# Optimization experiments

Measured on AMD Instinct MI355X. Metric: run time of the kernel, lower is better.

The kernel has to match this reference:

```python
import jax, jax.numpy as jnp
import numpy as np
import math

B, S, D, H = 2, 2048, 1024, 16
DH = D // H
DFF = 4 * D
EPS = 1e-6


def layer_norm(x, g, b):
    # Faithful to the torch module: std is Bessel-corrected (ddof=1) and eps is
    # added to std (not variance).
    mean = jnp.mean(x, axis=-1, keepdims=True)
    var = jnp.sum((x - mean) ** 2, axis=-1, keepdims=True) / (x.shape[-1] - 1)
    return g * (x - mean) / (jnp.sqrt(var) + EPS) + b


def gelu_tanh(h):
    c = math.sqrt(2.0 / math.pi)
    return 0.5 * h * (1.0 + jnp.tanh(c * (h + 0.044715 * h ** 3)))


def attention(x, mask, wq, bq, wk, bk, wv, bv, wo, bo):
    b, s, d = x.shape
    q = (x @ wq + bq).reshape(b, s, H, DH)
    k = (x @ wk + bk).reshape(b, s, H, DH)
    v = (x @ wv + bv).reshape(b, s, H, DH)
    corr = jnp.einsum('bqhd,bkhd->bhqk', q, k) / math.sqrt(DH)  # [B,H,S,S]
    # original builds mask[:,None,:].repeat -> key-axis padding mask
    corr = jnp.where(mask[:, None, None, :] == 0, jnp.float32(-1e9), corr)
    prob = jax.nn.softmax(corr, axis=-1)
    hid = jnp.einsum('bhqk,bkhd->bqhd', prob, v).reshape(b, s, d)
    return hid @ wo + bo


def setup_inputs() -> dict:
    key = jax.random.key(0)
    ks = jax.random.split(key, 16)
    std = 0.02
    inp = {
        'hidden': jax.random.normal(ks[0], (B, S, D), jnp.float32),
        'mask': jax.random.randint(ks[1], (B, S), 0, 2, jnp.int32),
        'wq': jax.random.normal(ks[2], (D, D), jnp.float32) * std,
        'bq': jnp.zeros((D,), jnp.float32),
        'wk': jax.random.normal(ks[3], (D, D), jnp.float32) * std,
        'bk': jnp.zeros((D,), jnp.float32),
        'wv': jax.random.normal(ks[4], (D, D), jnp.float32) * std,
        'bv': jnp.zeros((D,), jnp.float32),
        'wo': jax.random.normal(ks[5], (D, D), jnp.float32) * std,
        'bo': jnp.zeros((D,), jnp.float32),
        'w1': jax.random.normal(ks[6], (D, DFF), jnp.float32) * std,
        'b1': jnp.zeros((DFF,), jnp.float32),
        'w2': jax.random.normal(ks[7], (DFF, D), jnp.float32) * std,
        'b2': jnp.zeros((D,), jnp.float32),
        'ln1_g': jnp.ones((D,), jnp.float32),
        'ln1_b': jnp.zeros((D,), jnp.float32),
        'ln2_g': jnp.ones((D,), jnp.float32),
        'ln2_b': jnp.zeros((D,), jnp.float32),
    }
    return inp


def reference(hidden, mask, wq, bq, wk, bk, wv, bv, wo, bo, w1, b1, w2, b2,
              ln1_g, ln1_b, ln2_g, ln2_b):
    # pre-norm residual attention sublayer (dropout = identity in eval)
    h = hidden + attention(layer_norm(hidden, ln1_g, ln1_b), mask,
                           wq, bq, wk, bk, wv, bv, wo, bo)
    # pre-norm residual FFN sublayer with tanh-GELU
    ff_in = layer_norm(h, ln2_g, ln2_b)
    h = h + (gelu_tanh(ff_in @ w1 + b1) @ w2 + b2)
    return h
```

## Files before the change

### kernel.cpp

```cpp
#include <hip/hip_runtime.h>

#define BB 2
#define SS 2048
#define DD 1024
#define HH 16
#define DHH 64
#define DFF 4096
#define MM (BB * SS)

typedef unsigned short u16;
typedef short short8 __attribute__((ext_vector_type(8)));
typedef float f32x4 __attribute__((ext_vector_type(4)));

__device__ __forceinline__ float b2f(u16 u) {
    return __uint_as_float(((unsigned)u) << 16);
}
__device__ __forceinline__ u16 f2b(float f) {
    unsigned u = __float_as_uint(f);
    unsigned r = (u + 0x7fffu + ((u >> 16) & 1u)) >> 16;
    return (u16)r;
}
__device__ __forceinline__ float gelu_tanh_f(float x) {
    float x3 = x * x * x;
    float t = 0.7978845608028654f * (x + 0.044715f * x3);
    return 0.5f * x * (1.0f + tanhf(t));
}

__global__ __launch_bounds__(256) void wconv(const float* __restrict__ W,
                                             u16* __restrict__ WT,
                                             int Kdim, int Ndim) {
    __shared__ float tile[64][65];
    const int t = threadIdx.x;
    const int k0 = blockIdx.x * 64, n0 = blockIdx.y * 64;
    const int c = t & 63, r0 = (t >> 6) * 16;
#pragma unroll
    for (int i = 0; i < 16; ++i)
        tile[r0 + i][c] = W[(size_t)(k0 + r0 + i) * Ndim + n0 + c];
    __syncthreads();
    const int k4 = (t & 15) * 4, nr = t >> 4;
#pragma unroll
    for (int i = 0; i < 4; ++i) {
        int n = nr + 16 * i;
        ushort4 u = {f2b(tile[k4 + 0][n]), f2b(tile[k4 + 1][n]),
                     f2b(tile[k4 + 2][n]), f2b(tile[k4 + 3][n])};
        *(ushort4*)&WT[(size_t)(n0 + n) * Kdim + k0 + k4] = u;
    }
}

template <typename TI>
__global__ __launch_bounds__(256) void ln_kernel(const TI* __restrict__ x,
                                                 const float* __restrict__ g,
                                                 const float* __restrict__ bb,
                                                 u16* __restrict__ out) {
    __shared__ float red[8];
    const int row = blockIdx.x;
    const int t = threadIdx.x;
    const size_t base = (size_t)row * DD;

    float xv[4];
#pragma unroll
    for (int i = 0; i < 4; ++i) {
        int j = t + i * 256;
        if constexpr (sizeof(TI) == 2) xv[i] = b2f(((const u16*)x)[base + j]);
        else                            xv[i] = ((const float*)x)[base + j];
    }

    float part = xv[0] + xv[1] + xv[2] + xv[3];
#pragma unroll
    for (int off = 32; off > 0; off >>= 1) part += __shfl_xor(part, off);
    if ((t & 63) == 0) red[t >> 6] = part;
    __syncthreads();
    const float mean = (red[0] + red[1] + red[2] + red[3]) * (1.0f / 1024.0f);

    float dv[4];
#pragma unroll
    for (int i = 0; i < 4; ++i) dv[i] = xv[i] - mean;
    float p2 = dv[0] * dv[0] + dv[1] * dv[1] + dv[2] * dv[2] + dv[3] * dv[3];
#pragma unroll
    for (int off = 32; off > 0; off >>= 1) p2 += __shfl_xor(p2, off);
    if ((t & 63) == 0) red[4 + (t >> 6)] = p2;
    __syncthreads();
    const float var = (red[4] + red[5] + red[6] + red[7]) * (1.0f / 1023.0f);
    const float rden = 1.0f / (sqrtf(var) + 1e-6f);

#pragma unroll
    for (int i = 0; i < 4; ++i) {
        int j = t + i * 256;
        out[base + j] = f2b(g[j] * dv[i] * rden + bb[j]);
    }
}

template <int EPI>
__device__ __forceinline__ void gemm_store(int row, int col, float v,
                                           const void* res, void* out, int Ndim) {
    if (EPI == 0 || EPI == 4) {
        if (EPI == 4) v *= 0.125f;
        const int bq = row >> 11, ss = row & 2047;
        const int hh = col >> 6, dh = col & 63;
        ((u16*)out)[(((size_t)bq * HH + hh) * SS + ss) * DHH + dh] = f2b(v);
    } else if (EPI == 1) {
        const size_t o = (size_t)row * Ndim + col;
        ((u16*)out)[o] = f2b(v + ((const float*)res)[o]);
    } else if (EPI == 2) {
        ((u16*)out)[(size_t)row * Ndim + col] = f2b(gelu_tanh_f(v));
    } else {
        const size_t o = (size_t)row * Ndim + col;
        ((float*)out)[o] = v + b2f(((const u16*)res)[o]);
    }
}

template <int EPI, int TM>
__global__ __launch_bounds__(256) void gemm_bb(const u16* __restrict__ A,
                                               const u16* __restrict__ BTg,
                                               const float* __restrict__ bias,
                                               const void* __restrict__ res,
                                               void* __restrict__ out,
                                               int Ndim, int Kdim) {
    constexpr int NI = (TM == 128) ? 4 : 2;
    __shared__ __align__(16) u16 As[TM * 64];
    __shared__ __align__(16) u16 Bs[128 * 64];

    const int t = threadIdx.x;
    const int w = t >> 6, l = t & 63;
    const int lm = l & 15, lg = l >> 4;
    const int m0 = blockIdx.y * TM, n0 = blockIdx.x * 128;
    const int wro = (TM == 128) ? (w >> 1) * 64 : 0;
    const int wco = (TM == 128) ? (w & 1) * 64 : w * 32;

    f32x4 acc[4][NI];
#pragma unroll
    for (int mi = 0; mi < 4; ++mi)
#pragma unroll
        for (int ni = 0; ni < NI; ++ni) acc[mi][ni] = (f32x4){0.f, 0.f, 0.f, 0.f};

    for (int k0 = 0; k0 < Kdim; k0 += 64) {
#pragma unroll
        for (int it = 0; it < TM / 32; ++it) {
            int idx = it * 256 + t;
            int row = idx >> 3, c8 = (idx & 7) * 8;
            short8 v = *(const short8*)(A + (size_t)(m0 + row) * Kdim + k0 + c8);
            *(short8*)&As[row * 64 + (c8 ^ ((row & 7) * 8))] = v;
        }
#pragma unroll
        for (int it = 0; it < 4; ++it) {
            int idx = it * 256 + t;
            int row = idx >> 3, c8 = (idx & 7) * 8;
            short8 v = *(const short8*)(BTg + (size_t)(n0 + row) * Kdim + k0 + c8);
            *(short8*)&Bs[row * 64 + (c8 ^ ((row & 7) * 8))] = v;
        }
        __syncthreads();

#pragma unroll
        for (int ks = 0; ks < 64; ks += 32) {
            short8 af[4], bf[NI];
#pragma unroll
            for (int mi = 0; mi < 4; ++mi) {
                const int row = wro + mi * 16 + lm;
                af[mi] = *(const short8*)&As[row * 64 + ((ks + lg * 8) ^ ((row & 7) * 8))];
            }
#pragma unroll
            for (int ni = 0; ni < NI; ++ni) {
                const int nn = wco + ni * 16 + lm;
                bf[ni] = *(const short8*)&Bs[nn * 64 + ((ks + lg * 8) ^ ((nn & 7) * 8))];
            }
#pragma unroll
            for (int mi = 0; mi < 4; ++mi)
#pragma unroll
                for (int ni = 0; ni < NI; ++ni)
                    acc[mi][ni] = __builtin_amdgcn_mfma_f32_16x16x32_bf16(
                        af[mi], bf[ni], acc[mi][ni], 0, 0, 0);
        }
        __syncthreads();
    }

#pragma unroll
    for (int ni = 0; ni < NI; ++ni) {
        const int col = n0 + wco + ni * 16 + lm;
        const float bv = bias[col];
#pragma unroll
        for (int mi = 0; mi < 4; ++mi)
#pragma unroll
            for (int r = 0; r < 4; ++r)
                gemm_store<EPI>(m0 + wro + mi * 16 + lg * 4 + r, col,
                                acc[mi][ni][r] + bv, res, out, Ndim);
    }
}

template <int EPI, int TM>
__global__ __launch_bounds__(256) void gemm_fb(const u16* __restrict__ A,
                                               const float* __restrict__ W,
                                               const float* __restrict__ bias,
                                               const void* __restrict__ res,
                                               void* __restrict__ out,
                                               int Ndim, int Kdim) {
    constexpr int NI = (TM == 128) ? 4 : 2;
    __shared__ __align__(16) u16 As[TM * 64];
    __shared__ __align__(16) u16 BT[128 * 64];

    const int t = threadIdx.x;
    const int w = t >> 6, l = t & 63;
    const int lm = l & 15, lg = l >> 4;
    const int m0 = blockIdx.y * TM, n0 = blockIdx.x * 128;
    const int wro = (TM == 128) ? (w >> 1) * 64 : 0;
    const int wco = (TM == 128) ? (w & 1) * 64 : w * 32;

    f32x4 acc[4][NI];
#pragma unroll
    for (int mi = 0; mi < 4; ++mi)
#pragma unroll
        for (int ni = 0; ni < NI; ++ni) acc[mi][ni] = (f32x4){0.f, 0.f, 0.f, 0.f};

    const int bn = t & 127;
    const int bk4 = (t >> 7) * 4;

    for (int k0 = 0; k0 < Kdim; k0 += 64) {
#pragma unroll
        for (int it = 0; it < TM / 32; ++it) {
            int idx = it * 256 + t;
            int row = idx >> 3, c8 = (idx & 7) * 8;
            short8 v = *(const short8*)(A + (size_t)(m0 + row) * Kdim + k0 + c8);
            *(short8*)&As[row * 64 + (c8 ^ ((row & 7) * 8))] = v;
        }
#pragma unroll
        for (int it = 0; it < 8; ++it) {
            int kq = it * 8 + bk4;
            const float* wp = W + (size_t)(k0 + kq) * Ndim + n0 + bn;
            ushort4 u = {f2b(wp[0]), f2b(wp[(size_t)Ndim]),
                         f2b(wp[2 * (size_t)Ndim]), f2b(wp[3 * (size_t)Ndim])};
            *(ushort4*)&BT[bn * 64 + (kq ^ ((bn & 7) * 8))] = u;
        }
        __syncthreads();

#pragma unroll
        for (int ks = 0; ks < 64; ks += 32) {
            short8 af[4], bf[NI];
#pragma unroll
            for (int mi = 0; mi < 4; ++mi) {
                const int row = wro + mi * 16 + lm;
                af[mi] = *(const short8*)&As[row * 64 + ((ks + lg * 8) ^ ((row & 7) * 8))];
            }
#pragma unroll
            for (int ni = 0; ni < NI; ++ni) {
                const int nn = wco + ni * 16 + lm;
                bf[ni] = *(const short8*)&BT[nn * 64 + ((ks + lg * 8) ^ ((nn & 7) * 8))];
            }
#pragma unroll
            for (int mi = 0; mi < 4; ++mi)
#pragma unroll
                for (int ni = 0; ni < NI; ++ni)
                    acc[mi][ni] = __builtin_amdgcn_mfma_f32_16x16x32_bf16(
                        af[mi], bf[ni], acc[mi][ni], 0, 0, 0);
        }
        __syncthreads();
    }

#pragma unroll
    for (int ni = 0; ni < NI; ++ni) {
        const int col = n0 + wco + ni * 16 + lm;
        const float bv = bias[col];
#pragma unroll
        for (int mi = 0; mi < 4; ++mi)
#pragma unroll
            for (int r = 0; r < 4; ++r)
                gemm_store<EPI>(m0 + wro + mi * 16 + lg * 4 + r, col,
                                acc[mi][ni][r] + bv, res, out, Ndim);
    }
}

__global__ __launch_bounds__(256) void attn_mfma2(const u16* __restrict__ qg,
                                                  const u16* __restrict__ kg,
                                                  const u16* __restrict__ vg,
                                                  const int* __restrict__ mask,
                                                  u16* __restrict__ hid) {
    __shared__ __align__(16) u16 Ks[64 * 72];
    __shared__ __align__(16) u16 VTs[64 * 72];
    __shared__ __align__(16) float maskf[64];

    const int t = threadIdx.x;
    const int w = t >> 6;
    const int l = t & 63;
    const int lm = l & 15, lg = l >> 4;
    const int h = blockIdx.y, b = blockIdx.z;
    const int qbase = blockIdx.x * 128 + w * 32;
    const size_t bhS = ((size_t)b * HH + h) * SS;

    short8 qlo[2], qhi[2];
#pragma unroll
    for (int qp = 0; qp < 2; ++qp) {
        const u16* qrow = qg + (bhS + qbase + qp * 16 + lm) * DHH + lg * 8;
        qlo[qp] = *(const short8*)qrow;
        qhi[qp] = *(const short8*)(qrow + 32);
    }

    f32x4 acc[2][4];
#pragma unroll
    for (int qp = 0; qp < 2; ++qp)
#pragma unroll
        for (int i = 0; i < 4; ++i) acc[qp][i] = (f32x4){0.f, 0.f, 0.f, 0.f};
    float sume[2] = {0.f, 0.f};

    const int kq = (t & 15) * 4, dq = (t >> 4) * 4;

    for (int kt = 0; kt < SS; kt += 64) {
        __syncthreads();
#pragma unroll
        for (int it = 0; it < 4; ++it) {
            int idx = it * 256 + t;
            int row = idx >> 4, c4 = (idx & 15) * 4;
            ushort4 u = *(const ushort4*)(kg + (bhS + kt + row) * DHH + c4);
            *(ushort4*)&Ks[row * 72 + c4] = u;
        }
        {
            ushort4 a0 = *(const ushort4*)(vg + (bhS + kt + kq + 0) * DHH + dq);
            ushort4 a1 = *(const ushort4*)(vg + (bhS + kt + kq + 1) * DHH + dq);
            ushort4 a2 = *(const ushort4*)(vg + (bhS + kt + kq + 2) * DHH + dq);
            ushort4 a3 = *(const ushort4*)(vg + (bhS + kt + kq + 3) * DHH + dq);
            ushort4 w0 = {a0.x, a1.x, a2.x, a3.x};
            ushort4 w1 = {a0.y, a1.y, a2.y, a3.y};
            ushort4 w2 = {a0.z, a1.z, a2.z, a3.z};
            ushort4 w3 = {a0.w, a1.w, a2.w, a3.w};
            *(ushort4*)&VTs[(dq + 0) * 72 + kq] = w0;
            *(ushort4*)&VTs[(dq + 1) * 72 + kq] = w1;
            *(ushort4*)&VTs[(dq + 2) * 72 + kq] = w2;
            *(ushort4*)&VTs[(dq + 3) * 72 + kq] = w3;
        }
        if (t < 64) maskf[t] = mask[b * SS + kt + t] ? 1.0f : 0.0f;
        __syncthreads();

#pragma unroll
        for (int kb = 0; kb < 64; kb += 32) {
            short8 kfa[2], kfc[2];
#pragma unroll
            for (int s = 0; s < 2; ++s) {
                const int keyrow = kb + 8 * (lm >> 2) + 4 * s + (lm & 3);
                const u16* kr = &Ks[keyrow * 72 + lg * 8];
                kfa[s] = *(const short8*)kr;
                kfc[s] = *(const short8*)(kr + 32);
            }
            short8 p8[2];
#pragma unroll
            for (int qp = 0; qp < 2; ++qp) {
                float ev[8];
#pragma unroll
                for (int s = 0; s < 2; ++s) {
                    f32x4 c = (f32x4){0.f, 0.f, 0.f, 0.f};
                    c = __builtin_amdgcn_mfma_f32_16x16x32_bf16(kfa[s], qlo[qp], c, 0, 0, 0);
                    c = __builtin_amdgcn_mfma_f32_16x16x32_bf16(kfc[s], qhi[qp], c, 0, 0, 0);
                    const float4 mv = *(const float4*)&maskf[kb + 8 * lg + 4 * s];
                    float e0 = __expf(c[0]) * mv.x;
                    float e1 = __expf(c[1]) * mv.y;
                    float e2 = __expf(c[2]) * mv.z;
                    float e3 = __expf(c[3]) * mv.w;
                    sume[qp] += e0 + e1 + e2 + e3;
                    ev[4 * s + 0] = e0; ev[4 * s + 1] = e1;
                    ev[4 * s + 2] = e2; ev[4 * s + 3] = e3;
                }
#pragma unroll
                for (int i = 0; i < 8; ++i) p8[qp][i] = (short)f2b(ev[i]);
            }
#pragma unroll
            for (int d0 = 0; d0 < 4; ++d0) {
                const short8 v8 = *(const short8*)&VTs[(d0 * 16 + lm) * 72 + kb + lg * 8];
#pragma unroll
                for (int qp = 0; qp < 2; ++qp)
                    acc[qp][d0] = __builtin_amdgcn_mfma_f32_16x16x32_bf16(
                        p8[qp], v8, acc[qp][d0], 0, 0, 0);
            }
        }
    }

#pragma unroll
    for (int qp = 0; qp < 2; ++qp) {
        float s = sume[qp];
        s += __shfl_xor(s, 16);
        s += __shfl_xor(s, 32);
        float rinv[4];
#pragma unroll
        for (int r = 0; r < 4; ++r) rinv[r] = 1.0f / __shfl(s, 4 * lg + r);
#pragma unroll
        for (int d0 = 0; d0 < 4; ++d0)
#pragma unroll
            for (int r = 0; r < 4; ++r) {
                const int q = qbase + qp * 16 + 4 * lg + r;
                hid[(size_t)(b * SS + q) * DD + h * DHH + d0 * 16 + lm] =
                    f2b(acc[qp][d0][r] * rinv[r]);
            }
    }
}

extern "C" void kernel_launch(void* const* d_in, const int* in_sizes, int n_in,
                              void* d_out, int out_size, void* d_ws, size_t ws_size,
                              hipStream_t stream) {
    (void)in_sizes; (void)n_in; (void)out_size;

    const float* hidden = (const float*)d_in[0];
    const int*   mask   = (const int*)d_in[1];
    const float* wq = (const float*)d_in[2];  const float* bq = (const float*)d_in[3];
    const float* wk = (const float*)d_in[4];  const float* bk = (const float*)d_in[5];
    const float* wv = (const float*)d_in[6];  const float* bv = (const float*)d_in[7];
    const float* wo = (const float*)d_in[8];  const float* bo = (const float*)d_in[9];
    const float* w1 = (const float*)d_in[10]; const float* b1 = (const float*)d_in[11];
    const float* w2 = (const float*)d_in[12]; const float* b2 = (const float*)d_in[13];
    const float* ln1g = (const float*)d_in[14]; const float* ln1b = (const float*)d_in[15];
    const float* ln2g = (const float*)d_in[16]; const float* ln2b = (const float*)d_in[17];

    char* ws = (char*)d_ws;
    u16* R0 = (u16*)(ws + 0);
    u16* R1 = (u16*)(ws + 8388608);
    u16* R2 = (u16*)(ws + 16777216);
    u16* R3 = (u16*)(ws + 25165824);
    float* outp = (float*)d_out;

    const size_t WTOFF = 33554432;
    const bool big = ws_size >= WTOFF + 25165824;

    if (big) {
        u16* wqT = (u16*)(ws + WTOFF);
        u16* wkT = (u16*)(ws + WTOFF + 2097152);
        u16* wvT = (u16*)(ws + WTOFF + 4194304);
        u16* woT = (u16*)(ws + WTOFF + 6291456);
        u16* w1T = (u16*)(ws + WTOFF + 8388608);
        u16* w2T = (u16*)(ws + WTOFF + 16777216);

        wconv<<<dim3(DD / 64, DD / 64), 256, 0, stream>>>(wq, wqT, DD, DD);
        wconv<<<dim3(DD / 64, DD / 64), 256, 0, stream>>>(wk, wkT, DD, DD);
        wconv<<<dim3(DD / 64, DD / 64), 256, 0, stream>>>(wv, wvT, DD, DD);
        wconv<<<dim3(DD / 64, DD / 64), 256, 0, stream>>>(wo, woT, DD, DD);
        wconv<<<dim3(DD / 64, DFF / 64), 256, 0, stream>>>(w1, w1T, DD, DFF);
        wconv<<<dim3(DFF / 64, DD / 64), 256, 0, stream>>>(w2, w2T, DFF, DD);

        ln_kernel<float><<<MM, 256, 0, stream>>>(hidden, ln1g, ln1b, R0);
        gemm_bb<4, 128><<<dim3(DD / 128, MM / 128), 256, 0, stream>>>(R0, wqT, bq, nullptr, R1, DD, DD);
        gemm_bb<0, 128><<<dim3(DD / 128, MM / 128), 256, 0, stream>>>(R0, wkT, bk, nullptr, R2, DD, DD);
        gemm_bb<0, 128><<<dim3(DD / 128, MM / 128), 256, 0, stream>>>(R0, wvT, bv, nullptr, R3, DD, DD);
        attn_mfma2<<<dim3(SS / 128, HH, BB), 256, 0, stream>>>(R1, R2, R3, mask, R0);
        gemm_bb<1, 128><<<dim3(DD / 128, MM / 128), 256, 0, stream>>>(R0, woT, bo, hidden, R3, DD, DD);
        ln_kernel<u16><<<MM, 256, 0, stream>>>(R3, ln2g, ln2b, R0);
        for (int s2 = 0; s2 < 2; ++s2) {
            const size_t r0 = (size_t)s2 * 2048;
            gemm_bb<2, 128><<<dim3(DFF / 128, 2048 / 128), 256, 0, stream>>>(
                R0 + r0 * DD, w1T, b1, nullptr, R1, DFF, DD);
            gemm_bb<3, 64><<<dim3(DD / 128, 2048 / 64), 256, 0, stream>>>(
                R1, w2T, b2, R3 + r0 * DD, outp + r0 * DD, DD, DFF);
        }
    } else {
        ln_kernel<float><<<MM, 256, 0, stream>>>(hidden, ln1g, ln1b, R0);
        gemm_fb<4, 128><<<dim3(DD / 128, MM / 128), 256, 0, stream>>>(R0, wq, bq, nullptr, R1, DD, DD);
        gemm_fb<0, 128><<<dim3(DD / 128, MM / 128), 256, 0, stream>>>(R0, wk, bk, nullptr, R2, DD, DD);
        gemm_fb<0, 128><<<dim3(DD / 128, MM / 128), 256, 0, stream>>>(R0, wv, bv, nullptr, R3, DD, DD);
        attn_mfma2<<<dim3(SS / 128, HH, BB), 256, 0, stream>>>(R1, R2, R3, mask, R0);
        gemm_fb<1, 128><<<dim3(DD / 128, MM / 128), 256, 0, stream>>>(R0, wo, bo, hidden, R3, DD, DD);
        ln_kernel<u16><<<MM, 256, 0, stream>>>(R3, ln2g, ln2b, R0);
        for (int s2 = 0; s2 < 2; ++s2) {
            const size_t r0 = (size_t)s2 * 2048;
            gemm_fb<2, 128><<<dim3(DFF / 128, 2048 / 128), 256, 0, stream>>>(
                R0 + r0 * DD, w1, b1, nullptr, R1, DFF, DD);
            gemm_fb<3, 64><<<dim3(DD / 128, 2048 / 64), 256, 0, stream>>>(
                R1, w2, b2, R3 + r0 * DD, outp + r0 * DD, DD, DFF);
        }
    }
}
```

Before: 531.7 us.

## Fuse QKV projections into one GEMM and load tiles via global_load_lds

Concatenates the transposed Q/K/V weights and biases so a single GEMM with a new epilogue writes Q (scaled), K and V into three head-major regions, replacing three launches. GEMM tile staging now uses direct global-to-LDS 16-byte loads with the XOR swizzle moved to the source address, skipping the register round trip. Attention probabilities are converted to bf16 by truncation instead of round-to-nearest, which saves ALU work at a small accuracy cost. The fused path relies on R1/R2/R3 being contiguous 8 MB regions, matching the 4194304-element region stride.

```diff
diff --git a/kernel.cpp b/kernel.cpp
--- a/kernel.cpp
+++ b/kernel.cpp
@@ -25,6 +25,11 @@
     float t = 0.7978845608028654f * (x + 0.044715f * x3);
     return 0.5f * x * (1.0f + tanhf(t));
 }
+__device__ __forceinline__ void cp16(const u16* g, u16* l) {
+    __builtin_amdgcn_global_load_lds(
+        (const __attribute__((address_space(1))) void*)g,
+        (__attribute__((address_space(3))) void*)l, 16, 0, 0);
+}
 
 __global__ __launch_bounds__(256) void wconv(const float* __restrict__ W,
                                              u16* __restrict__ WT,
@@ -45,6 +50,14 @@
                      f2b(tile[k4 + 2][n]), f2b(tile[k4 + 3][n])};
         *(ushort4*)&WT[(size_t)(n0 + n) * Kdim + k0 + k4] = u;
     }
+}
+
+__global__ __launch_bounds__(256) void pack3(const float* __restrict__ a,
+                                             const float* __restrict__ b,
+                                             const float* __restrict__ c,
+                                             float* __restrict__ o) {
+    int i = blockIdx.x * 256 + threadIdx.x;
+    o[i] = (i < 1024) ? a[i] : ((i < 2048) ? b[i - 1024] : c[i - 2048]);
 }
 
 template <typename TI>
@@ -98,6 +111,13 @@
         const int bq = row >> 11, ss = row & 2047;
         const int hh = col >> 6, dh = col & 63;
         ((u16*)out)[(((size_t)bq * HH + hh) * SS + ss) * DHH + dh] = f2b(v);
+    } else if (EPI == 5) {
+        const int reg = col >> 10, cc = col & 1023;
+        if (reg == 0) v *= 0.125f;
+        const int bq = row >> 11, ss = row & 2047;
+        const int hh = cc >> 6, dh = cc & 63;
+        ((u16*)out)[(size_t)reg * 4194304 +
+                    (((size_t)bq * HH + hh) * SS + ss) * DHH + dh] = f2b(v);
     } else if (EPI == 1) {
         const size_t o = (size_t)row * Ndim + col;
         ((u16*)out)[o] = f2b(v + ((const float*)res)[o]);
@@ -110,13 +130,14 @@
 }
 
 template <int EPI, int TM>
-__global__ __launch_bounds__(256) void gemm_bb(const u16* __restrict__ A,
+__global__ __launch_bounds__(256) void gemm_as(const u16* __restrict__ A,
                                                const u16* __restrict__ BTg,
                                                const float* __restrict__ bias,
                                                const void* __restrict__ res,
                                                void* __restrict__ out,
                                                int Ndim, int Kdim) {
     constexpr int NI = (TM == 128) ? 4 : 2;
+    constexpr int NCA = TM / 32;
     __shared__ __align__(16) u16 As[TM * 64];
     __shared__ __align__(16) u16 Bs[128 * 64];
 
@@ -135,18 +156,18 @@
 
     for (int k0 = 0; k0 < Kdim; k0 += 64) {
 #pragma unroll
-        for (int it = 0; it < TM / 32; ++it) {
-            int idx = it * 256 + t;
-            int row = idx >> 3, c8 = (idx & 7) * 8;
-            short8 v = *(const short8*)(A + (size_t)(m0 + row) * Kdim + k0 + c8);
-            *(short8*)&As[row * 64 + (c8 ^ ((row & 7) * 8))] = v;
-        }
-#pragma unroll
-        for (int it = 0; it < 4; ++it) {
-            int idx = it * 256 + t;
-            int row = idx >> 3, c8 = (idx & 7) * 8;
-            short8 v = *(const short8*)(BTg + (size_t)(n0 + row) * Kdim + k0 + c8);
-            *(short8*)&Bs[row * 64 + (c8 ^ ((row & 7) * 8))] = v;
+        for (int j = 0; j < NCA; ++j) {
+            const int c = (w * NCA + j) * 64 + l;
+            const int r = c >> 3, g = (c & 7) ^ (r & 7);
+            cp16(A + (size_t)(m0 + r) * Kdim + k0 + g * 8,
+                 &As[(w * NCA + j) * 512]);
+        }
+#pragma unroll
+        for (int j = 0; j < 4; ++j) {
+            const int c = (w * 4 + j) * 64 + l;
+            const int r = c >> 3, g = (c & 7) ^ (r & 7);
+            cp16(BTg + (size_t)(n0 + r) * Kdim + k0 + g * 8,
+                 &Bs[(w * 4 + j) * 512]);
         }
         __syncthreads();
 
@@ -356,7 +377,8 @@
                     ev[4 * s + 2] = e2; ev[4 * s + 3] = e3;
                 }
 #pragma unroll
-                for (int i = 0; i < 8; ++i) p8[qp][i] = (short)f2b(ev[i]);
+                for (int i = 0; i < 8; ++i)
+                    p8[qp][i] = (short)(__float_as_uint(ev[i]) >> 16);
             }
 #pragma unroll
             for (int d0 = 0; d0 < 4; ++d0) {
@@ -412,35 +434,35 @@
     float* outp = (float*)d_out;
 
     const size_t WTOFF = 33554432;
-    const bool big = ws_size >= WTOFF + 25165824;
+    const bool big = ws_size >= WTOFF + 25165824 + 16384;
 
     if (big) {
-        u16* wqT = (u16*)(ws + WTOFF);
-        u16* wkT = (u16*)(ws + WTOFF + 2097152);
-        u16* wvT = (u16*)(ws + WTOFF + 4194304);
-        u16* woT = (u16*)(ws + WTOFF + 6291456);
-        u16* w1T = (u16*)(ws + WTOFF + 8388608);
-        u16* w2T = (u16*)(ws + WTOFF + 16777216);
-
-        wconv<<<dim3(DD / 64, DD / 64), 256, 0, stream>>>(wq, wqT, DD, DD);
-        wconv<<<dim3(DD / 64, DD / 64), 256, 0, stream>>>(wk, wkT, DD, DD);
-        wconv<<<dim3(DD / 64, DD / 64), 256, 0, stream>>>(wv, wvT, DD, DD);
+        u16* qkvT = (u16*)(ws + WTOFF);
+        u16* woT  = (u16*)(ws + WTOFF + 6291456);
+        u16* w1T  = (u16*)(ws + WTOFF + 8388608);
+        u16* w2T  = (u16*)(ws + WTOFF + 16777216);
+        float* bqkv = (float*)(ws + WTOFF + 25165824);
+
+        wconv<<<dim3(DD / 64, DD / 64), 256, 0, stream>>>(wq, qkvT, DD, DD);
+        wconv<<<dim3(DD / 64, DD / 64), 256, 0, stream>>>(wk, qkvT + (size_t)1024 * DD, DD, DD);
+        wconv<<<dim3(DD / 64, DD / 64), 256, 0, stream>>>(wv, qkvT + (size_t)2048 * DD, DD, DD);
         wconv<<<dim3(DD / 64, DD / 64), 256, 0, stream>>>(wo, woT, DD, DD);
         wconv<<<dim3(DD / 64, DFF / 64), 256, 0, stream>>>(w1, w1T, DD, DFF);
         wconv<<<dim3(DFF / 64, DD / 64), 256, 0, stream>>>(w2, w2T, DFF, DD);
+        pack3<<<12, 256, 0, stream>>>(bq, bk, bv, bqkv);
 
         ln_kernel<float><<<MM, 256, 0, stream>>>(hidden, ln1g, ln1b, R0);
-        gemm_bb<4, 128><<<dim3(DD / 128, MM / 128), 256, 0, stream>>>(R0, wqT, bq, nullptr, R1, DD, DD);
-        gemm_bb<0, 128><<<dim3(DD / 128, MM / 128), 256, 0, stream>>>(R0, wkT, bk, nullptr, R2, DD, DD);
-        gemm_bb<0, 128><<<dim3(DD / 128, MM / 128), 256, 0, stream>>>(R0, wvT, bv, nullptr, R3, DD, DD);
+        gemm_as<5, 128><<<dim3(3072 / 128, MM / 128), 256, 0, stream>>>(
+            R0, qkvT, bqkv, nullptr, R1, 3072, DD);
         attn_mfma2<<<dim3(SS / 128, HH, BB), 256, 0, stream>>>(R1, R2, R3, mask, R0);
-        gemm_bb<1, 128><<<dim3(DD / 128, MM / 128), 256, 0, stream>>>(R0, woT, bo, hidden, R3, DD, DD);
+        gemm_as<1, 128><<<dim3(DD / 128, MM / 128), 256, 0, stream>>>(
+            R0, woT, bo, hidden, R3, DD, DD);
         ln_kernel<u16><<<MM, 256, 0, stream>>>(R3, ln2g, ln2b, R0);
         for (int s2 = 0; s2 < 2; ++s2) {
             const size_t r0 = (size_t)s2 * 2048;
-            gemm_bb<2, 128><<<dim3(DFF / 128, 2048 / 128), 256, 0, stream>>>(
+            gemm_as<2, 128><<<dim3(DFF / 128, 2048 / 128), 256, 0, stream>>>(
                 R0 + r0 * DD, w1T, b1, nullptr, R1, DFF, DD);
-            gemm_bb<3, 64><<<dim3(DD / 128, 2048 / 64), 256, 0, stream>>>(
+            gemm_as<3, 64><<<dim3(DD / 128, 2048 / 64), 256, 0, stream>>>(
                 R1, w2T, b2, R3 + r0 * DD, outp + r0 * DD, DD, DFF);
         }
     } else {
```

New measurement: 491.3 us. 1.08x faster.
